# Performance work log

Measured on AMD Instinct MI355X. Metric: run time of the kernel, lower is better.

## Reference

```python
import jax, jax.numpy as jnp
import numpy as np

N = 20000   # nodes
K = 32      # neighbors per node (kNN graph)
C = 128     # input feature dim
H = 256     # h_theta hidden/output dim
E = N * K   # edges


def setup_inputs() -> dict:
    key = jax.random.key(0)
    k1, k2, k3, k4 = jax.random.split(key, 4)
    node_features = jax.random.normal(k1, (N, C), dtype=jnp.float32)
    senders = jax.random.randint(k2, (E,), 0, N)              # neighbor node per edge
    receivers = jnp.repeat(jnp.arange(N), K)                  # center node per edge (k-NN: exactly K each)
    W1 = jax.random.normal(k3, (2 * C, H), dtype=jnp.float32) * (1.0 / np.sqrt(2 * C))
    b1 = jnp.zeros((H,), dtype=jnp.float32)
    W2 = jax.random.normal(k4, (H, H), dtype=jnp.float32) * (1.0 / np.sqrt(H))
    b2 = jnp.zeros((H,), dtype=jnp.float32)
    return {"node_features": node_features, "senders": senders, "receivers": receivers,
            "W1": W1, "b1": b1, "W2": W2, "b2": b2}


def reference(node_features, senders, receivers, W1, b1, W2, b2):
    # gather: x_v (center) and x_vp (neighbor) per edge -> [E, C]
    x_v = node_features[receivers]
    x_vp = node_features[senders]
    # edge feature: concat([x_v, x_vp - x_v]) -> [E, 2C]
    e = jnp.concatenate([x_v, x_vp - x_v], axis=-1)
    # h_theta MLP per edge -> [E, H]
    h = jnp.dot(jax.nn.relu(jnp.dot(e, W1) + b1), W2) + b2
    # max-reduce over each node's incident edges -> [N, H]
    return jax.ops.segment_max(h, receivers, num_segments=N)
```

## Files before the change

kernel.cpp:

```cpp
#include <hip/hip_runtime.h>
#include <hip/hip_bf16.h>

#define NN    20000
#define KNN   32
#define CIN   128
#define HD    256
#define EE    (NN * KNN)
#define MT    64
#define TPB   10
#define NBLK  (EE / (MT * TPB))
#define YSTR  264

typedef __bf16 bf16x8_t __attribute__((ext_vector_type(8)));
typedef __bf16 bf16x4_t __attribute__((ext_vector_type(4)));
typedef float  f32x4_t  __attribute__((ext_vector_type(4)));

__device__ __forceinline__ void gload_lds16(const __bf16* g, __bf16* l) {
    __builtin_amdgcn_global_load_lds(
        (const __attribute__((address_space(1))) void*)g,
        (__attribute__((address_space(3))) void*)l, 16, 0, 0);
}

__global__ void ec_prep(const float* __restrict__ nf, const float* __restrict__ W1,
                        const float* __restrict__ W2, __bf16* __restrict__ nfb,
                        __bf16* __restrict__ w1g, __bf16* __restrict__ w2t) {
    int bid = blockIdx.x;
    if (bid < (NN * CIN) / 1024) {
        int i = (bid * 256 + threadIdx.x) * 4;
        float4 v = *(const float4*)(nf + i);
        bf16x4_t b = { (__bf16)v.x, (__bf16)v.y, (__bf16)v.z, (__bf16)v.w };
        *(bf16x4_t*)(nfb + i) = b;
    } else {
        int idx = (bid - (NN * CIN) / 1024) * 256 + threadIdx.x;
        int k = idx >> 8, n = idx & 255;
        float v = (k < CIN) ? (W1[k * 256 + n] - W1[(k + CIN) * 256 + n])
                            : W1[k * 256 + n];
        int kt = k >> 5, qr = (k >> 3) & 3, j = k & 7;
        w1g[(size_t)((kt * 4 + qr) * 256 + n) * 8 + j] = (__bf16)v;
        w2t[n * 256 + k] = (__bf16)W2[k * 256 + n];
    }
}

__global__ __launch_bounds__(512, 1) void ec_main(
    const __bf16* __restrict__ nfb,
    const int*   __restrict__ senders,
    const __bf16* __restrict__ w1g,
    const __bf16* __restrict__ w2t,
    const float* __restrict__ b1,
    const float* __restrict__ b2,
    float* __restrict__ out)
{
    __shared__ __attribute__((aligned(16))) __bf16 ldsW[16384];
    __shared__ __attribute__((aligned(16))) __bf16 ldsE[2][8192];
    __shared__ __attribute__((aligned(16))) __bf16 ldsH[16384];
    __shared__ __attribute__((aligned(16))) __bf16 ldsY[20 * YSTR];

    const int tid  = threadIdx.x;
    const int lane = tid & 63;
    const int wave = tid >> 6;
    const int qrow = lane >> 4;
    const int lcol = lane & 15;
    const int blk  = blockIdx.x;
    const int fsl  = wave * 32;
    const int fs2  = (wave >> 1) * 64;
    const int eh   = wave & 1;
    const int p0 = wave * 2, p1 = wave * 2 + 1;
    const int c0 = p0 >> 2, q0 = p0 & 3;
    const int c1 = p1 >> 2, q1 = p1 & 3;

    {
        const float4* src = (const float4*)(w1g + 49152);
        float4* dst = (float4*)ldsW;
#pragma unroll
        for (int i = 0; i < 4; ++i)
            dst[i * 512 + tid] = src[i * 512 + tid];
    }

    {
        int s0 = senders[blk * TPB * MT + lane];
        gload_lds16(nfb + (size_t)s0 * CIN + c0 * 32 + q0 * 8, &ldsE[0][p0 * 512]);
        gload_lds16(nfb + (size_t)s0 * CIN + c1 * 32 + q1 * 8, &ldsE[0][p1 * 512]);
    }

    {
        f32x4_t ay[2][2];
#pragma unroll
        for (int mi = 0; mi < 2; ++mi)
#pragma unroll
            for (int ni = 0; ni < 2; ++ni)
                ay[mi][ni] = (f32x4_t){0.f, 0.f, 0.f, 0.f};
        bf16x8_t xv[2][4];
#pragma unroll
        for (int ni = 0; ni < 2; ++ni) {
            int ln = ni * 16 + lcol; if (ln > 19) ln = 19;
            const __bf16* row = nfb + (size_t)(blk * 20 + ln) * CIN;
#pragma unroll
            for (int c = 0; c < 4; ++c)
                xv[ni][c] = *(const bf16x8_t*)(row + c * 32 + qrow * 8);
        }
#pragma unroll
        for (int kt = 0; kt < 4; ++kt) {
            bf16x8_t wy[2];
#pragma unroll
            for (int mi = 0; mi < 2; ++mi)
                wy[mi] = *(const bf16x8_t*)(w1g +
                    (size_t)((kt * 4 + qrow) * 256 + fsl + mi * 16 + lcol) * 8);
#pragma unroll
            for (int mi = 0; mi < 2; ++mi)
#pragma unroll
                for (int ni = 0; ni < 2; ++ni)
                    ay[mi][ni] = __builtin_amdgcn_mfma_f32_16x16x32_bf16(
                        wy[mi], xv[ni][kt], ay[mi][ni], 0, 0, 0);
        }
#pragma unroll
        for (int mi = 0; mi < 2; ++mi)
#pragma unroll
            for (int ni = 0; ni < 2; ++ni) {
                int ln = ni * 16 + lcol;
                if (ln < 20) {
                    bf16x4_t yb = { (__bf16)ay[mi][ni][0], (__bf16)ay[mi][ni][1],
                                    (__bf16)ay[mi][ni][2], (__bf16)ay[mi][ni][3] };
                    *(bf16x4_t*)(ldsY + ln * YSTR + fsl + mi * 16 + qrow * 4) = yb;
                }
            }
    }

    bf16x8_t w1s[2][2];
#pragma unroll
    for (int s = 0; s < 2; ++s)
#pragma unroll
        for (int mi = 0; mi < 2; ++mi)
            w1s[s][mi] = *(const bf16x8_t*)(w1g +
                (size_t)(((4 + s) * 4 + qrow) * 256 + fsl + mi * 16 + lcol) * 8);

    bf16x8_t w2f[8][4];
#pragma unroll
    for (int kt = 0; kt < 8; ++kt)
#pragma unroll
        for (int ni = 0; ni < 4; ++ni)
            w2f[kt][ni] = *(const bf16x8_t*)(w2t + (size_t)(fs2 + ni * 16 + lcol) * 256
                                                 + kt * 32 + qrow * 8);

    float4 bias1[2];
#pragma unroll
    for (int mi = 0; mi < 2; ++mi)
        bias1[mi] = *(const float4*)(b1 + fsl + mi * 16 + qrow * 4);
    float bias2[4];
#pragma unroll
    for (int ni = 0; ni < 4; ++ni)
        bias2[ni] = b2[fs2 + ni * 16 + lcol];

    __syncthreads();

#pragma unroll 1
    for (int t = 0; t < TPB; ++t) {
        const int node0 = (blk * TPB + t) * 2;
        const int cur = t & 1;

        if (t + 1 < TPB) {
            int sN = senders[(blk * TPB + t + 1) * MT + lane];
            const __bf16* srow = nfb + (size_t)sN * CIN;
            gload_lds16(srow + c0 * 32 + q0 * 8, &ldsE[1 - cur][p0 * 512]);
            gload_lds16(srow + c1 * 32 + q1 * 8, &ldsE[1 - cur][p1 * 512]);
        }

        f32x4_t acc[2][4];
#pragma unroll
        for (int mi = 0; mi < 2; ++mi)
#pragma unroll
            for (int ni = 0; ni < 4; ++ni) {
                bf16x4_t yb = *(const bf16x4_t*)(ldsY + (t * 2 + (ni >> 1)) * YSTR
                                                 + fsl + mi * 16 + qrow * 4);
                acc[mi][ni] = (f32x4_t){ (float)yb[0], (float)yb[1],
                                         (float)yb[2], (float)yb[3] };
            }
#pragma unroll
        for (int kt = 0; kt < 4; ++kt) {
            bf16x8_t wf[2], ef[4];
#pragma unroll
            for (int mi = 0; mi < 2; ++mi) {
                if (kt < 2) wf[mi] = w1s[kt][mi];
                else        wf[mi] = *(const bf16x8_t*)(ldsW +
                    (size_t)(((kt - 2) * 4 + qrow) * 256 + fsl + mi * 16 + lcol) * 8);
            }
#pragma unroll
            for (int ni = 0; ni < 4; ++ni)
                ef[ni] = *(const bf16x8_t*)(&ldsE[cur][0] +
                    (size_t)((kt * 4 + qrow) * 64 + ni * 16 + lcol) * 8);
#pragma unroll
            for (int mi = 0; mi < 2; ++mi)
#pragma unroll
                for (int ni = 0; ni < 4; ++ni)
                    acc[mi][ni] = __builtin_amdgcn_mfma_f32_16x16x32_bf16(
                        wf[mi], ef[ni], acc[mi][ni], 0, 0, 0);
        }

        __syncthreads();

#pragma unroll
        for (int mi = 0; mi < 2; ++mi) {
            const int f0  = fsl + mi * 16 + qrow * 4;
            const int ktp = f0 >> 5, qrp = (f0 >> 3) & 3, jh = f0 & 7;
            float4 bb = bias1[mi];
#pragma unroll
            for (int ni = 0; ni < 4; ++ni) {
                int edge = ni * 16 + lcol;
                float v0 = acc[mi][ni][0] + bb.x;
                float v1 = acc[mi][ni][1] + bb.y;
                float v2 = acc[mi][ni][2] + bb.z;
                float v3 = acc[mi][ni][3] + bb.w;
                bf16x4_t h = { (__bf16)fmaxf(v0, 0.f), (__bf16)fmaxf(v1, 0.f),
                               (__bf16)fmaxf(v2, 0.f), (__bf16)fmaxf(v3, 0.f) };
                *(bf16x4_t*)(ldsH + (size_t)((ktp * 4 + qrp) * 64 + edge) * 8 + jh) = h;
            }
        }
        __syncthreads();

        f32x4_t acc2[2][4];
#pragma unroll
        for (int mi = 0; mi < 2; ++mi)
#pragma unroll
            for (int ni = 0; ni < 4; ++ni)
                acc2[mi][ni] = (f32x4_t){0.f, 0.f, 0.f, 0.f};
#pragma unroll
        for (int kt = 0; kt < 8; ++kt) {
            bf16x8_t af[2];
#pragma unroll
            for (int mi = 0; mi < 2; ++mi)
                af[mi] = *(const bf16x8_t*)(ldsH +
                    (size_t)((kt * 4 + qrow) * 64 + eh * 32 + mi * 16 + lcol) * 8);
#pragma unroll
            for (int mi = 0; mi < 2; ++mi)
#pragma unroll
                for (int ni = 0; ni < 4; ++ni)
                    acc2[mi][ni] = __builtin_amdgcn_mfma_f32_16x16x32_bf16(
                        af[mi], w2f[kt][ni], acc2[mi][ni], 0, 0, 0);
        }

#pragma unroll
        for (int ni = 0; ni < 4; ++ni) {
            int col = fs2 + ni * 16 + lcol;
            float mx = -3.402823466e38f;
#pragma unroll
            for (int mi = 0; mi < 2; ++mi)
#pragma unroll
                for (int r = 0; r < 4; ++r)
                    mx = fmaxf(mx, acc2[mi][ni][r]);
            mx = fmaxf(mx, __shfl_xor(mx, 16, 64));
            mx = fmaxf(mx, __shfl_xor(mx, 32, 64));
            if (qrow == 0)
                out[(size_t)(node0 + eh) * HD + col] = mx + bias2[ni];
        }
    }
}

extern "C" void kernel_launch(void* const* d_in, const int* in_sizes, int n_in,
                              void* d_out, int out_size, void* d_ws, size_t ws_size,
                              hipStream_t stream) {
    const float* nf      = (const float*)d_in[0];
    const int*   senders = (const int*)d_in[1];
    const float* W1 = (const float*)d_in[3];
    const float* b1 = (const float*)d_in[4];
    const float* W2 = (const float*)d_in[5];
    const float* b2 = (const float*)d_in[6];

    __bf16* w1g = (__bf16*)d_ws;
    __bf16* w2t = w1g + 256 * 256;
    __bf16* nfb = w2t + 256 * 256;

    ec_prep<<<(NN * CIN) / 1024 + 256, 256, 0, stream>>>(nf, W1, W2, nfb, w1g, w2t);
    ec_main<<<NBLK, 512, 0, stream>>>(nfb, senders, w1g, w2t, b1, b2, (float*)d_out);
}
```

Before: 241.3 us.

## Software-pipeline the two MLP GEMMs and raise occupancy to two blocks

Restructures the per-tile loop so the second GEMM for tile t-1 runs in the same iteration as the first GEMM for tile t, using a double-buffered hidden-activation LDS buffer. This drops one barrier per iteration. W2 is re-laid-out into the same fragment-blocked format as W1, with its last k-slice moved to LDS so fewer registers are needed. Launch bounds change to allow two 512-thread blocks per CU. LDS use grows (about 135KB per block), which may prevent two blocks from fitting, and register pressure could cause spills under the tighter bound.

New measurement: 230.1 us. -4.6%, faster.

```diff
diff --git a/kernel.cpp b/kernel.cpp
--- a/kernel.cpp
+++ b/kernel.cpp
@@ -23,7 +23,7 @@
 
 __global__ void ec_prep(const float* __restrict__ nf, const float* __restrict__ W1,
                         const float* __restrict__ W2, __bf16* __restrict__ nfb,
-                        __bf16* __restrict__ w1g, __bf16* __restrict__ w2t) {
+                        __bf16* __restrict__ w1g, __bf16* __restrict__ w2g) {
     int bid = blockIdx.x;
     if (bid < (NN * CIN) / 1024) {
         int i = (bid * 256 + threadIdx.x) * 4;
@@ -33,26 +33,28 @@
     } else {
         int idx = (bid - (NN * CIN) / 1024) * 256 + threadIdx.x;
         int k = idx >> 8, n = idx & 255;
-        float v = (k < CIN) ? (W1[k * 256 + n] - W1[(k + CIN) * 256 + n])
-                            : W1[k * 256 + n];
+        float v1 = (k < CIN) ? (W1[k * 256 + n] - W1[(k + CIN) * 256 + n])
+                             : W1[k * 256 + n];
         int kt = k >> 5, qr = (k >> 3) & 3, j = k & 7;
-        w1g[(size_t)((kt * 4 + qr) * 256 + n) * 8 + j] = (__bf16)v;
-        w2t[n * 256 + k] = (__bf16)W2[k * 256 + n];
+        size_t off = (size_t)((kt * 4 + qr) * 256 + n) * 8 + j;
+        w1g[off] = (__bf16)v1;
+        w2g[off] = (__bf16)W2[k * 256 + n];
     }
 }
 
-__global__ __launch_bounds__(512, 1) void ec_main(
+__global__ __launch_bounds__(512, 2) void ec_main(
     const __bf16* __restrict__ nfb,
     const int*   __restrict__ senders,
     const __bf16* __restrict__ w1g,
-    const __bf16* __restrict__ w2t,
+    const __bf16* __restrict__ w2g,
     const float* __restrict__ b1,
     const float* __restrict__ b2,
     float* __restrict__ out)
 {
-    __shared__ __attribute__((aligned(16))) __bf16 ldsW[16384];
+    __shared__ __attribute__((aligned(16))) __bf16 ldsW1s[16384];
+    __shared__ __attribute__((aligned(16))) __bf16 ldsW27[8192];
     __shared__ __attribute__((aligned(16))) __bf16 ldsE[2][8192];
-    __shared__ __attribute__((aligned(16))) __bf16 ldsH[16384];
+    __shared__ __attribute__((aligned(16))) __bf16 ldsH[2][16384];
     __shared__ __attribute__((aligned(16))) __bf16 ldsY[20 * YSTR];
 
     const int tid  = threadIdx.x;
@@ -69,11 +71,14 @@
     const int c1 = p1 >> 2, q1 = p1 & 3;
 
     {
-        const float4* src = (const float4*)(w1g + 49152);
-        float4* dst = (float4*)ldsW;
-#pragma unroll
-        for (int i = 0; i < 4; ++i)
-            dst[i * 512 + tid] = src[i * 512 + tid];
+        const float4* s1 = (const float4*)(w1g + 49152);
+        float4* d1 = (float4*)ldsW1s;
+#pragma unroll
+        for (int i = 0; i < 4; ++i) d1[i * 512 + tid] = s1[i * 512 + tid];
+        const float4* s2 = (const float4*)(w2g + 57344);
+        float4* d2 = (float4*)ldsW27;
+#pragma unroll
+        for (int i = 0; i < 2; ++i) d2[i * 512 + tid] = s2[i * 512 + tid];
     }
 
     {
@@ -133,13 +138,24 @@
             w1s[s][mi] = *(const bf16x8_t*)(w1g +
                 (size_t)(((4 + s) * 4 + qrow) * 256 + fsl + mi * 16 + lcol) * 8);
 
-    bf16x8_t w2f[8][4];
-#pragma unroll
-    for (int kt = 0; kt < 8; ++kt)
+    bf16x8_t w2f[7][4];
+#pragma unroll
+    for (int kt = 0; kt < 7; ++kt)
 #pragma unroll
         for (int ni = 0; ni < 4; ++ni)
-            w2f[kt][ni] = *(const bf16x8_t*)(w2t + (size_t)(fs2 + ni * 16 + lcol) * 256
-                                                 + kt * 32 + qrow * 8);
+            w2f[kt][ni] = *(const bf16x8_t*)(w2g +
+                (size_t)((kt * 4 + qrow) * 256 + fs2 + ni * 16 + lcol) * 8);
+
+#pragma unroll
+    for (int s = 0; s < 2; ++s)
+#pragma unroll
+        for (int mi = 0; mi < 2; ++mi)
+            asm volatile("" : "+v"(w1s[s][mi]));
+#pragma unroll
+    for (int kt = 0; kt < 7; ++kt)
+#pragma unroll
+        for (int ni = 0; ni < 4; ++ni)
+            asm volatile("" : "+v"(w2f[kt][ni]));
 
     float4 bias1[2];
 #pragma unroll
@@ -153,103 +169,116 @@
     __syncthreads();
 
 #pragma unroll 1
-    for (int t = 0; t < TPB; ++t) {
-        const int node0 = (blk * TPB + t) * 2;
+    for (int t = 0; t <= TPB; ++t) {
         const int cur = t & 1;
-
-        if (t + 1 < TPB) {
-            int sN = senders[(blk * TPB + t + 1) * MT + lane];
-            const __bf16* srow = nfb + (size_t)sN * CIN;
-            gload_lds16(srow + c0 * 32 + q0 * 8, &ldsE[1 - cur][p0 * 512]);
-            gload_lds16(srow + c1 * 32 + q1 * 8, &ldsE[1 - cur][p1 * 512]);
-        }
-
         f32x4_t acc[2][4];
-#pragma unroll
-        for (int mi = 0; mi < 2; ++mi)
+
+        if (t < TPB) {
+            if (t + 1 < TPB) {
+                int sN = senders[(blk * TPB + t + 1) * MT + lane];
+                const __bf16* srow = nfb + (size_t)sN * CIN;
+                gload_lds16(srow + c0 * 32 + q0 * 8, &ldsE[1 - cur][p0 * 512]);
+                gload_lds16(srow + c1 * 32 + q1 * 8, &ldsE[1 - cur][p1 * 512]);
+            }
+
+#pragma unroll
+            for (int mi = 0; mi < 2; ++mi)
+#pragma unroll
+                for (int ni = 0; ni < 4; ++ni) {
+                    bf16x4_t yb = *(const bf16x4_t*)(ldsY + (t * 2 + (ni >> 1)) * YSTR
+                                                     + fsl + mi * 16 + qrow * 4);
+                    acc[mi][ni] = (f32x4_t){ (float)yb[0], (float)yb[1],
+                                             (float)yb[2], (float)yb[3] };
+                }
+#pragma unroll
+            for (int kt = 0; kt < 4; ++kt) {
+                bf16x8_t wf[2], ef[4];
+#pragma unroll
+                for (int mi = 0; mi < 2; ++mi) {
+                    if (kt < 2) wf[mi] = w1s[kt][mi];
+                    else        wf[mi] = *(const bf16x8_t*)(ldsW1s +
+                        (size_t)(((kt - 2) * 4 + qrow) * 256 + fsl + mi * 16 + lcol) * 8);
+                }
+#pragma unroll
+                for (int ni = 0; ni < 4; ++ni)
+                    ef[ni] = *(const bf16x8_t*)(&ldsE[cur][0] +
+                        (size_t)((kt * 4 + qrow) * 64 + ni * 16 + lcol) * 8);
+#pragma unroll
+                for (int mi = 0; mi < 2; ++mi)
+#pragma unroll
+                    for (int ni = 0; ni < 4; ++ni)
+                        acc[mi][ni] = __builtin_amdgcn_mfma_f32_16x16x32_bf16(
+                            wf[mi], ef[ni], acc[mi][ni], 0, 0, 0);
+            }
+        }
+
+        __syncthreads();
+
+        if (t < TPB) {
+#pragma unroll
+            for (int mi = 0; mi < 2; ++mi) {
+                const int f0  = fsl + mi * 16 + qrow * 4;
+                const int ktp = f0 >> 5, qrp = (f0 >> 3) & 3, jh = f0 & 7;
+                float4 bb = bias1[mi];
+#pragma unroll
+                for (int ni = 0; ni < 4; ++ni) {
+                    int edge = ni * 16 + lcol;
+                    float v0 = acc[mi][ni][0] + bb.x;
+                    float v1 = acc[mi][ni][1] + bb.y;
+                    float v2 = acc[mi][ni][2] + bb.z;
+                    float v3 = acc[mi][ni][3] + bb.w;
+                    bf16x4_t h = { (__bf16)fmaxf(v0, 0.f), (__bf16)fmaxf(v1, 0.f),
+                                   (__bf16)fmaxf(v2, 0.f), (__bf16)fmaxf(v3, 0.f) };
+                    *(bf16x4_t*)(&ldsH[cur][0] +
+                        (size_t)((ktp * 4 + qrp) * 64 + edge) * 8 + jh) = h;
+                }
+            }
+        }
+
+        if (t > 0) {
+            const __bf16* Hp = &ldsH[1 - cur][0];
+            f32x4_t acc2[2][4];
+#pragma unroll
+            for (int mi = 0; mi < 2; ++mi)
+#pragma unroll
+                for (int ni = 0; ni < 4; ++ni)
+                    acc2[mi][ni] = (f32x4_t){0.f, 0.f, 0.f, 0.f};
+#pragma unroll
+            for (int kt = 0; kt < 8; ++kt) {
+                bf16x8_t af[2], wf[4];
+#pragma unroll
+                for (int mi = 0; mi < 2; ++mi)
+                    af[mi] = *(const bf16x8_t*)(Hp +
+                        (size_t)((kt * 4 + qrow) * 64 + eh * 32 + mi * 16 + lcol) * 8);
+#pragma unroll
+                for (int ni = 0; ni < 4; ++ni) {
+                    if (kt < 7) wf[ni] = w2f[kt][ni];
+                    else        wf[ni] = *(const bf16x8_t*)(ldsW27 +
+                        (size_t)(qrow * 256 + fs2 + ni * 16 + lcol) * 8);
+                }
+#pragma unroll
+                for (int mi = 0; mi < 2; ++mi)
+#pragma unroll
+                    for (int ni = 0; ni < 4; ++ni)
+                        acc2[mi][ni] = __builtin_amdgcn_mfma_f32_16x16x32_bf16(
+                            af[mi], wf[ni], acc2[mi][ni], 0, 0, 0);
+            }
+
+            const int node0p = (blk * TPB + t - 1) * 2;
 #pragma unroll
             for (int ni = 0; ni < 4; ++ni) {
-                bf16x4_t yb = *(const bf16x4_t*)(ldsY + (t * 2 + (ni >> 1)) * YSTR
-                                                 + fsl + mi * 16 + qrow * 4);
-                acc[mi][ni] = (f32x4_t){ (float)yb[0], (float)yb[1],
-                                         (float)yb[2], (float)yb[3] };
-            }
-#pragma unroll
-        for (int kt = 0; kt < 4; ++kt) {
-            bf16x8_t wf[2], ef[4];
-#pragma unroll
-            for (int mi = 0; mi < 2; ++mi) {
-                if (kt < 2) wf[mi] = w1s[kt][mi];
-                else        wf[mi] = *(const bf16x8_t*)(ldsW +
-                    (size_t)(((kt - 2) * 4 + qrow) * 256 + fsl + mi * 16 + lcol) * 8);
-            }
-#pragma unroll
-            for (int ni = 0; ni < 4; ++ni)
-                ef[ni] = *(const bf16x8_t*)(&ldsE[cur][0] +
-                    (size_t)((kt * 4 + qrow) * 64 + ni * 16 + lcol) * 8);
-#pragma unroll
-            for (int mi = 0; mi < 2; ++mi)
-#pragma unroll
-                for (int ni = 0; ni < 4; ++ni)
-                    acc[mi][ni] = __builtin_amdgcn_mfma_f32_16x16x32_bf16(
-                        wf[mi], ef[ni], acc[mi][ni], 0, 0, 0);
-        }
-
-        __syncthreads();
-
-#pragma unroll
-        for (int mi = 0; mi < 2; ++mi) {
-            const int f0  = fsl + mi * 16 + qrow * 4;
-            const int ktp = f0 >> 5, qrp = (f0 >> 3) & 3, jh = f0 & 7;
-            float4 bb = bias1[mi];
-#pragma unroll
-            for (int ni = 0; ni < 4; ++ni) {
-                int edge = ni * 16 + lcol;
-                float v0 = acc[mi][ni][0] + bb.x;
-                float v1 = acc[mi][ni][1] + bb.y;
-                float v2 = acc[mi][ni][2] + bb.z;
-                float v3 = acc[mi][ni][3] + bb.w;
-                bf16x4_t h = { (__bf16)fmaxf(v0, 0.f), (__bf16)fmaxf(v1, 0.f),
-                               (__bf16)fmaxf(v2, 0.f), (__bf16)fmaxf(v3, 0.f) };
-                *(bf16x4_t*)(ldsH + (size_t)((ktp * 4 + qrp) * 64 + edge) * 8 + jh) = h;
-            }
-        }
-        __syncthreads();
-
-        f32x4_t acc2[2][4];
-#pragma unroll
-        for (int mi = 0; mi < 2; ++mi)
-#pragma unroll
-            for (int ni = 0; ni < 4; ++ni)
-                acc2[mi][ni] = (f32x4_t){0.f, 0.f, 0.f, 0.f};
-#pragma unroll
-        for (int kt = 0; kt < 8; ++kt) {
-            bf16x8_t af[2];
-#pragma unroll
-            for (int mi = 0; mi < 2; ++mi)
-                af[mi] = *(const bf16x8_t*)(ldsH +
-                    (size_t)((kt * 4 + qrow) * 64 + eh * 32 + mi * 16 + lcol) * 8);
-#pragma unroll
-            for (int mi = 0; mi < 2; ++mi)
-#pragma unroll
-                for (int ni = 0; ni < 4; ++ni)
-                    acc2[mi][ni] = __builtin_amdgcn_mfma_f32_16x16x32_bf16(
-                        af[mi], w2f[kt][ni], acc2[mi][ni], 0, 0, 0);
-        }
-
-#pragma unroll
-        for (int ni = 0; ni < 4; ++ni) {
-            int col = fs2 + ni * 16 + lcol;
-            float mx = -3.402823466e38f;
-#pragma unroll
-            for (int mi = 0; mi < 2; ++mi)
-#pragma unroll
-                for (int r = 0; r < 4; ++r)
-                    mx = fmaxf(mx, acc2[mi][ni][r]);
-            mx = fmaxf(mx, __shfl_xor(mx, 16, 64));
-            mx = fmaxf(mx, __shfl_xor(mx, 32, 64));
-            if (qrow == 0)
-                out[(size_t)(node0 + eh) * HD + col] = mx + bias2[ni];
+                int col = fs2 + ni * 16 + lcol;
+                float mx = -3.402823466e38f;
+#pragma unroll
+                for (int mi = 0; mi < 2; ++mi)
+#pragma unroll
+                    for (int r = 0; r < 4; ++r)
+                        mx = fmaxf(mx, acc2[mi][ni][r]);
+                mx = fmaxf(mx, __shfl_xor(mx, 16, 64));
+                mx = fmaxf(mx, __shfl_xor(mx, 32, 64));
+                if (qrow == 0)
+                    out[(size_t)(node0p + eh) * HD + col] = mx + bias2[ni];
+            }
         }
     }
 }
@@ -265,9 +294,9 @@
     const float* b2 = (const float*)d_in[6];
 
     __bf16* w1g = (__bf16*)d_ws;
-    __bf16* w2t = w1g + 256 * 256;
-    __bf16* nfb = w2t + 256 * 256;
-
-    ec_prep<<<(NN * CIN) / 1024 + 256, 256, 0, stream>>>(nf, W1, W2, nfb, w1g, w2t);
-    ec_main<<<NBLK, 512, 0, stream>>>(nfb, senders, w1g, w2t, b1, b2, (float*)d_out);
+    __bf16* w2g = w1g + 256 * 256;
+    __bf16* nfb = w2g + 256 * 256;
+
+    ec_prep<<<(NN * CIN) / 1024 + 256, 256, 0, stream>>>(nf, W1, W2, nfb, w1g, w2g);
+    ec_main<<<NBLK, 512, 0, stream>>>(nfb, senders, w1g, w2g, b1, b2, (float*)d_out);
 }
```
